# Kernel tuning notes

Measured on AMD Instinct MI355X. Metric: run time of the kernel, lower is better.

Reference implementation:

```python
import jax, jax.numpy as jnp
import numpy as np

B, N, D_IN, D_OUT, H, W = 2, 2048, 1024, 1024, 16, 64
DH = D_OUT // H


def setup_inputs() -> dict:
    key = jax.random.key(0)
    ks = jax.random.split(key, 6)
    x = jax.random.normal(ks[0], (B, N, D_IN), dtype=jnp.float32)
    s_in = 1.0 / np.sqrt(D_IN)
    s_out = 1.0 / np.sqrt(D_OUT)
    wq = jax.random.normal(ks[1], (D_IN, D_OUT), dtype=jnp.float32) * s_in
    wk = jax.random.normal(ks[2], (D_IN, D_OUT), dtype=jnp.float32) * s_in
    wv = jax.random.normal(ks[3], (D_IN, D_OUT), dtype=jnp.float32) * s_in
    wo = jax.random.normal(ks[4], (D_OUT, D_OUT), dtype=jnp.float32) * s_out
    # sparse global tokens: every 256th token is global
    global_attention = (jnp.arange(N)[None, :] % 256 == 0) & jnp.ones((B, 1), bool)
    return {"x": x, "wq": wq, "wk": wk, "wv": wv, "wo": wo,
            "global_attention": global_attention}


def _mask(global_attention):
    # True = masked out. Causal local window + global rows/cols unmasked.
    i = jnp.arange(N)[:, None]
    j = jnp.arange(N)[None, :]
    allowed = (i - j < W) & (i >= j)          # causal sliding window
    local_mask = ~allowed                      # [N, N], True = masked
    g = global_attention                       # [B, N] bool
    # global token j clears row j and column j of the mask
    global_clear = g[:, :, None] | g[:, None, :]   # [B, N, N]
    return local_mask[None, :, :] & ~global_clear  # [B, N, N]


def reference(x, wq, wk, wv, wo, global_attention):
    b, n, _ = x.shape
    q = (x @ wq).reshape(b, n, H, DH).transpose(0, 2, 1, 3)  # [b,h,n,dh]
    k = (x @ wk).reshape(b, n, H, DH).transpose(0, 2, 1, 3)
    v = (x @ wv).reshape(b, n, H, DH).transpose(0, 2, 1, 3)
    scores = jnp.einsum('bhqd,bhkd->bhqk', q, k) / jnp.sqrt(jnp.float32(DH))
    mask = _mask(global_attention)[:, None, :, :]            # [b,1,n,n]
    scores = jnp.where(mask, -jnp.inf, scores)
    attn = jax.nn.softmax(scores, axis=-1)
    ctx = jnp.einsum('bhqk,bhkd->bqhd', attn, v).reshape(b, n, D_OUT)
    return ctx @ wo
```

## Files before the change

### kernel.cpp

```cpp
#include <hip/hip_runtime.h>


using u16 = unsigned short;
using u32 = unsigned int;

typedef __attribute__((ext_vector_type(8))) short bf16x8;
typedef __attribute__((ext_vector_type(4))) float f32x4;

__device__ __forceinline__ float b2f(u16 s) {
  union { u32 u; float f; } x; x.u = ((u32)s) << 16; return x.f;
}
__device__ __forceinline__ u16 f2b(float f) {
  union { float f; u32 u; } x; x.f = f;
  u32 r = (x.u + 0x7fffu + ((x.u >> 16) & 1u)) >> 16;
  return (u16)r;
}

__global__ __launch_bounds__(256) void k_pre(const float* __restrict__ x,
                                             u16* __restrict__ xb,
                                             const float* __restrict__ wq,
                                             const float* __restrict__ wk,
                                             const float* __restrict__ wv,
                                             const float* __restrict__ wo,
                                             u16* __restrict__ wqkvT,
                                             u16* __restrict__ woT) {
  __shared__ float tile[64][65];
  const int bid = blockIdx.x;
  if (bid < 2048) {
    int idx = (bid * 256 + threadIdx.x) * 8;
    float4 a = *(const float4*)(x + idx);
    float4 b = *(const float4*)(x + idx + 4);
    uint4 o;
    o.x = (u32)f2b(a.x) | ((u32)f2b(a.y) << 16);
    o.y = (u32)f2b(a.z) | ((u32)f2b(a.w) << 16);
    o.z = (u32)f2b(b.x) | ((u32)f2b(b.y) << 16);
    o.w = (u32)f2b(b.z) | ((u32)f2b(b.w) << 16);
    *(uint4*)(xb + idx) = o;
  } else {
    const int id = bid - 2048;
    const int z = id >> 8, xy = id & 255;
    const float* src = (z == 0) ? wq : (z == 1) ? wk : (z == 2) ? wv : wo;
    u16* dst = (z < 3) ? (wqkvT + ((size_t)z << 20)) : woT;
    const int n0 = (xy & 15) * 64, k0 = (xy >> 4) * 64;
    const int tx = threadIdx.x & 63, ty = threadIdx.x >> 6;
    #pragma unroll
    for (int r = 0; r < 64; r += 4)
      tile[r + ty][tx] = src[(size_t)(k0 + r + ty) * 1024 + n0 + tx];
    __syncthreads();
    #pragma unroll
    for (int r = 0; r < 64; r += 4)
      dst[(size_t)(n0 + r + ty) * 1024 + k0 + tx] = f2b(tile[tx][r + ty]);
  }
}

__device__ __forceinline__ void gload16(const u16* g, u16* l) {
  __builtin_amdgcn_global_load_lds((const __attribute__((address_space(1))) void*)g,
                                   (__attribute__((address_space(3))) void*)l, 16, 0, 0);
}

template<int F32OUT>
__global__ __launch_bounds__(256, 3) void k_gemm128(const u16* __restrict__ A,
                                                    const u16* __restrict__ Bt,
                                                    void* __restrict__ C, int N, int K) {
  __shared__ u16 lds[3][2][4096];
  const int t = threadIdx.x;
  const int wid = t >> 6, lane = t & 63;
  const int l4 = lane >> 4, l16 = lane & 15;
  const int wr = wid >> 1, wc = wid & 1;
  const int d = blockIdx.y * gridDim.x + blockIdx.x;
  const int qq = (gridDim.x * gridDim.y) >> 3;
  const int tau = (d & 7) * qq + (d >> 3);
  const int bn = tau % gridDim.x, bm = tau / gridDim.x;
  const u16* Ab = A + (size_t)bm * 128 * K;
  const u16* Bb = Bt + (size_t)bn * 128 * K;
  const int srow0 = t >> 2;
  const int scol = (((t & 3) ^ ((t >> 3) & 3)) << 3);
  const int sdst = wid << 9;
  const int sl8 = ((l4 ^ ((l16 >> 1) & 3)) << 3);
  const int NT = K >> 5;
  f32x4 acc[4][4] = {};

  #pragma unroll
  for (int pt = 0; pt < 2; ++pt) {
    #pragma unroll
    for (int c = 0; c < 2; ++c) {
      int r = c * 64 + srow0;
      gload16(Ab + (size_t)r * K + (pt << 5) + scol, &lds[pt][0][c * 2048 + sdst]);
      gload16(Bb + (size_t)r * K + (pt << 5) + scol, &lds[pt][1][c * 2048 + sdst]);
    }
  }

  int cur = 0, nxt2 = 2;
  for (int tt = 0; tt < NT; ++tt) {
    if (tt + 1 < NT) asm volatile("s_waitcnt vmcnt(4)" ::: "memory");
    else             asm volatile("s_waitcnt vmcnt(0)" ::: "memory");
    __builtin_amdgcn_s_barrier();
    if (tt + 2 < NT) {
      const int k0 = (tt + 2) << 5;
      u16* dA = &lds[nxt2][0][sdst];
      u16* dB = &lds[nxt2][1][sdst];
      #pragma unroll
      for (int c = 0; c < 2; ++c) {
        int r = c * 64 + srow0;
        gload16(Ab + (size_t)r * K + k0 + scol, dA + c * 2048);
        gload16(Bb + (size_t)r * K + k0 + scol, dB + c * 2048);
      }
    }
    const u16* As = lds[cur][0];
    const u16* Bs = lds[cur][1];
    bf16x8 af[4], bf[4];
    #pragma unroll
    for (int m = 0; m < 4; ++m)
      af[m] = *(const bf16x8*)&As[(wr * 64 + m * 16 + l16) * 32 + sl8];
    #pragma unroll
    for (int n = 0; n < 4; ++n)
      bf[n] = *(const bf16x8*)&Bs[(wc * 64 + n * 16 + l16) * 32 + sl8];
    __builtin_amdgcn_s_setprio(1);
    #pragma unroll
    for (int m = 0; m < 4; ++m)
      #pragma unroll
      for (int n = 0; n < 4; ++n)
        acc[m][n] = __builtin_amdgcn_mfma_f32_16x16x32_bf16(af[m], bf[n], acc[m][n], 0, 0, 0);
    __builtin_amdgcn_s_setprio(0);
    cur = (cur == 2) ? 0 : cur + 1;
    nxt2 = (nxt2 == 2) ? 0 : nxt2 + 1;
  }

  #pragma unroll
  for (int m = 0; m < 4; ++m) {
    const int row0 = bm * 128 + wr * 64 + m * 16 + l4 * 4;
    #pragma unroll
    for (int n = 0; n < 4; ++n) {
      const int col = bn * 128 + wc * 64 + n * 16 + l16;
      #pragma unroll
      for (int r = 0; r < 4; ++r) {
        if (F32OUT) ((float*)C)[(size_t)(row0 + r) * N + col] = acc[m][n][r];
        else        ((u16*)C)[(size_t)(row0 + r) * N + col] = f2b(acc[m][n][r]);
      }
    }
  }
}

template<int F32OUT>
__global__ __launch_bounds__(256, 2) void k_gemm64(const u16* __restrict__ A,
                                                   const u16* __restrict__ Bt,
                                                   void* __restrict__ C, int N, int K) {
  __shared__ u16 lds[3][6144];
  const int t = threadIdx.x;
  const int wid = t >> 6, lane = t & 63;
  const int l4 = lane >> 4, l16 = lane & 15;
  const int wr = wid >> 1, wc = wid & 1;
  const int d = blockIdx.y * gridDim.x + blockIdx.x;
  const int qq = (gridDim.x * gridDim.y) >> 3;
  const int tau = (d & 7) * qq + (d >> 3);
  const int bn = tau % gridDim.x, bm = tau / gridDim.x;
  const u16* Ab = A + (size_t)bm * 64 * K;
  const u16* Bb = Bt + (size_t)bn * 128 * K;
  const int srow0 = t >> 2;
  const int scol = (((t & 3) ^ ((t >> 3) & 3)) << 3);
  const int sdst = wid << 9;
  const int sl8 = ((l4 ^ ((l16 >> 1) & 3)) << 3);
  const int NT = K >> 5;
  f32x4 acc[2][4] = {};

  #pragma unroll
  for (int pt = 0; pt < 2; ++pt) {
    gload16(Ab + (size_t)srow0 * K + (pt << 5) + scol, &lds[pt][sdst]);
    #pragma unroll
    for (int c = 0; c < 2; ++c)
      gload16(Bb + (size_t)(c * 64 + srow0) * K + (pt << 5) + scol,
              &lds[pt][2048 + c * 2048 + sdst]);
  }

  int cur = 0, nxt2 = 2;
  for (int tt = 0; tt < NT; ++tt) {
    if (tt + 1 < NT) asm volatile("s_waitcnt vmcnt(3)" ::: "memory");
    else             asm volatile("s_waitcnt vmcnt(0)" ::: "memory");
    __builtin_amdgcn_s_barrier();
    if (tt + 2 < NT) {
      const int k0 = (tt + 2) << 5;
      u16* dst = &lds[nxt2][0];
      gload16(Ab + (size_t)srow0 * K + k0 + scol, dst + sdst);
      #pragma unroll
      for (int c = 0; c < 2; ++c)
        gload16(Bb + (size_t)(c * 64 + srow0) * K + k0 + scol, dst + 2048 + c * 2048 + sdst);
    }
    const u16* As = lds[cur];
    const u16* Bs = lds[cur] + 2048;
    bf16x8 af[2], bf[4];
    #pragma unroll
    for (int m = 0; m < 2; ++m)
      af[m] = *(const bf16x8*)&As[(wr * 32 + m * 16 + l16) * 32 + sl8];
    #pragma unroll
    for (int n = 0; n < 4; ++n)
      bf[n] = *(const bf16x8*)&Bs[(wc * 64 + n * 16 + l16) * 32 + sl8];
    __builtin_amdgcn_s_setprio(1);
    #pragma unroll
    for (int m = 0; m < 2; ++m)
      #pragma unroll
      for (int n = 0; n < 4; ++n)
        acc[m][n] = __builtin_amdgcn_mfma_f32_16x16x32_bf16(af[m], bf[n], acc[m][n], 0, 0, 0);
    __builtin_amdgcn_s_setprio(0);
    cur = (cur == 2) ? 0 : cur + 1;
    nxt2 = (nxt2 == 2) ? 0 : nxt2 + 1;
  }

  #pragma unroll
  for (int m = 0; m < 2; ++m) {
    const int row0 = bm * 64 + wr * 32 + m * 16 + l4 * 4;
    #pragma unroll
    for (int n = 0; n < 4; ++n) {
      const int col = bn * 128 + wc * 64 + n * 16 + l16;
      #pragma unroll
      for (int r = 0; r < 4; ++r) {
        if (F32OUT) ((float*)C)[(size_t)(row0 + r) * N + col] = acc[m][n][r];
        else        ((u16*)C)[(size_t)(row0 + r) * N + col] = f2b(acc[m][n][r]);
      }
    }
  }
}

__global__ __launch_bounds__(256) void k_attn_tile(const u16* __restrict__ qkv,
                                                   u16* __restrict__ ctx,
                                                   float* __restrict__ gpart) {
  __shared__ u16 buf[26880];
  __shared__ u16 Qgs[16 * 72];
  __shared__ u16 Pgs[16 * 72];
  __shared__ float lred[4][16];
  u16* Qs = buf;
  u16* Ks = buf + 4608;
  u16* Vt = buf + 16128;
  u16* Ps = buf;

  const int t = threadIdx.x, wid = t >> 6, lane = t & 63;
  const int l4 = lane >> 4, l16 = lane & 15;
  const int qt = blockIdx.x, h = blockIdx.y, b = blockIdx.z;
  const int q0 = qt * 64;
  const int kbase = q0 - 64;
  const size_t base = (size_t)b * 2048 * 3072;
  const u16* Qg = qkv + base + h * 64;
  const u16* Kg = qkv + base + 1024 + h * 64;
  const u16* Vg = qkv + base + 2048 + h * 64;

  for (int s = t; s < 512; s += 256) {
    int r = s >> 3, c = (s & 7) * 8;
    *(uint4*)&Qs[r * 72 + c] = *(const uint4*)&Qg[(size_t)(q0 + r) * 3072 + c];
  }
  if (t < 128) {
    int r = t >> 3, c = (t & 7) * 8;
    if (r < 8) {
      *(uint4*)&Qgs[r * 72 + c] = *(const uint4*)&Qg[(size_t)(r * 256) * 3072 + c];
    } else {
      uint4 z = {0, 0, 0, 0};
      *(uint4*)&Qgs[r * 72 + c] = z;
    }
  }
  for (int s = t; s < 1088; s += 256) {
    int r = s >> 3, c = (s & 7) * 8;
    int j = (r < 128) ? max(kbase + r, 0) : (r - 128) * 256;
    *(uint4*)&Ks[r * 72 + c] = *(const uint4*)&Kg[(size_t)j * 3072 + c];
  }
  for (int s = t; s < 1088; s += 256) {
    int r = s >> 3, c = (s & 7) * 8;
    int j = (r < 128) ? max(kbase + r, 0) : (r - 128) * 256;
    uint4 v = *(const uint4*)&Vg[(size_t)j * 3072 + c];
    const u16* pv = (const u16*)&v;
    #pragma unroll
    for (int e8 = 0; e8 < 8; ++e8) Vt[(c + e8) * 168 + r] = pv[e8];
  }
  for (int z = t; z < 64 * 24; z += 256) {
    int d = z / 24, j = 136 + z % 24;
    Vt[d * 168 + j] = 0;
  }
  __syncthreads();

  f32x4 sa[10] = {};
  #pragma unroll
  for (int ks = 0; ks < 2; ++ks) {
    bf16x8 qa = *(const bf16x8*)&Qs[(wid * 16 + l16) * 72 + ks * 32 + l4 * 8];
    #pragma unroll
    for (int n = 0; n < 10; ++n) {
      bf16x8 kb = *(const bf16x8*)&Ks[(n * 16 + l16) * 72 + ks * 32 + l4 * 8];
      sa[n] = __builtin_amdgcn_mfma_f32_16x16x32_bf16(qa, kb, sa[n], 0, 0, 0);
    }
  }

  f32x4 sg = {};
  #pragma unroll
  for (int ks = 0; ks < 2; ++ks) {
    bf16x8 qa = *(const bf16x8*)&Qgs[l16 * 72 + ks * 32 + l4 * 8];
    bf16x8 kb = *(const bf16x8*)&Ks[(64 + wid * 16 + l16) * 72 + ks * 32 + l4 * 8];
    sg = __builtin_amdgcn_mfma_f32_16x16x32_bf16(qa, kb, sg, 0, 0, 0);
  }
  #pragma unroll
  for (int r = 0; r < 4; ++r) {
    float p = __expf(sg[r] * 0.125f);
    sg[r] = p;
    #pragma unroll
    for (int o = 1; o < 16; o <<= 1) p += __shfl_xor(p, o);
    if (l16 == 0) lred[wid][l4 * 4 + r] = p;
  }
  #pragma unroll
  for (int r = 0; r < 4; ++r)
    Pgs[(l4 * 4 + r) * 72 + wid * 16 + l16] = f2b(sg[r]);

  const int qi0 = wid * 16 + l4 * 4;
  #pragma unroll
  for (int n = 0; n < 10; ++n) {
    const int jc = n * 16 + l16;
    #pragma unroll
    for (int r = 0; r < 4; ++r) {
      const int qi = qi0 + r;
      bool allowed;
      if (n < 8) {
        const int kr = kbase + jc;
        allowed = (jc > qi) && (jc <= qi + 64) && (kr >= 0) && ((kr & 255) != 0);
      } else {
        allowed = (jc < 136);
      }
      sa[n][r] = allowed ? sa[n][r] * 0.125f : -1e30f;
    }
  }

  float m[4], l[4];
  #pragma unroll
  for (int r = 0; r < 4; ++r) {
    float mx = sa[0][r];
    #pragma unroll
    for (int n = 1; n < 10; ++n) mx = fmaxf(mx, sa[n][r]);
    #pragma unroll
    for (int o = 1; o < 16; o <<= 1) mx = fmaxf(mx, __shfl_xor(mx, o));
    m[r] = mx;
    l[r] = 0.f;
  }
  #pragma unroll
  for (int n = 0; n < 10; ++n)
    #pragma unroll
    for (int r = 0; r < 4; ++r) {
      float p = __expf(sa[n][r] - m[r]);
      sa[n][r] = p;
      l[r] += p;
    }
  #pragma unroll
  for (int r = 0; r < 4; ++r)
    #pragma unroll
    for (int o = 1; o < 16; o <<= 1) l[r] += __shfl_xor(l[r], o);

  __syncthreads();

  u16* Pw = Ps + wid * (16 * 168);
  #pragma unroll
  for (int n = 0; n < 10; ++n)
    #pragma unroll
    for (int r = 0; r < 4; ++r)
      Pw[(l4 * 4 + r) * 168 + n * 16 + l16] = f2b(sa[n][r]);
  __builtin_amdgcn_wave_barrier();

  f32x4 o[4] = {};
  #pragma unroll
  for (int ks = 0; ks < 5; ++ks) {
    bf16x8 pa = *(const bf16x8*)&Pw[l16 * 168 + ks * 32 + l4 * 8];
    #pragma unroll
    for (int dt = 0; dt < 4; ++dt) {
      bf16x8 vb = *(const bf16x8*)&Vt[(dt * 16 + l16) * 168 + ks * 32 + l4 * 8];
      o[dt] = __builtin_amdgcn_mfma_f32_16x16x32_bf16(pa, vb, o[dt], 0, 0, 0);
    }
  }

  f32x4 og = {};
  #pragma unroll
  for (int ks = 0; ks < 2; ++ks) {
    bf16x8 pa = *(const bf16x8*)&Pgs[l16 * 72 + ks * 32 + l4 * 8];
    bf16x8 vb = *(const bf16x8*)&Vt[(wid * 16 + l16) * 168 + 64 + ks * 32 + l4 * 8];
    og = __builtin_amdgcn_mfma_f32_16x16x32_bf16(pa, vb, og, 0, 0, 0);
  }
  float* gp = gpart + ((size_t)(b * 16 + h) * 32 + qt) * 520;
  #pragma unroll
  for (int r = 0; r < 4; ++r) {
    int row = l4 * 4 + r;
    if (row < 8) gp[row * 64 + wid * 16 + l16] = og[r];
  }
  if (t < 8) gp[512 + t] = lred[0][t] + lred[1][t] + lred[2][t] + lred[3][t];

  #pragma unroll
  for (int r = 0; r < 4; ++r) {
    const int q = q0 + qi0 + r;
    if ((q & 255) == 0) continue;
    const float inv = 1.0f / l[r];
    #pragma unroll
    for (int dt = 0; dt < 4; ++dt)
      ctx[(size_t)(b * 2048 + q) * 1024 + h * 64 + dt * 16 + l16] = f2b(o[dt][r] * inv);
  }
}

__global__ __launch_bounds__(256) void k_attn_gred(const float* __restrict__ gpart,
                                                   u16* __restrict__ ctx) {
  const int bh = blockIdx.x;
  const int b = bh >> 4, h = bh & 15;
  const float* gp0 = gpart + (size_t)bh * 32 * 520;
  for (int s = threadIdx.x; s < 512; s += 256) {
    int row = s >> 6, d = s & 63;
    float o = 0.f, l = 0.f;
    for (int q = 0; q < 32; ++q) {
      o += gp0[q * 520 + s];
      l += gp0[q * 520 + 512 + row];
    }
    ctx[(size_t)(b * 2048 + row * 256) * 1024 + h * 64 + d] = f2b(o / l);
  }
}

extern "C" void kernel_launch(void* const* d_in, const int* in_sizes, int n_in,
                              void* d_out, int out_size, void* d_ws, size_t ws_size,
                              hipStream_t stream) {
  (void)in_sizes; (void)n_in; (void)out_size; (void)ws_size;
  const float* x  = (const float*)d_in[0];
  const float* wq = (const float*)d_in[1];
  const float* wk = (const float*)d_in[2];
  const float* wv = (const float*)d_in[3];
  const float* wo = (const float*)d_in[4];
  char* ws = (char*)d_ws;
  u16* xb    = (u16*)(ws);
  u16* qkv   = (u16*)(ws + (8u  << 20));
  u16* ctx   = (u16*)(ws + (32u << 20));
  u16* wqkvT = (u16*)(ws + (40u << 20));
  u16* woT   = (u16*)(ws + (46u << 20));
  float* gpart = (float*)(ws);

  k_pre<<<3072, 256, 0, stream>>>(x, xb, wq, wk, wv, wo, wqkvT, woT);
  k_gemm128<0><<<dim3(24, 32), 256, 0, stream>>>(xb, wqkvT, qkv, 3072, 1024);
  k_attn_tile<<<dim3(32, 16, 2), 256, 0, stream>>>(qkv, ctx, gpart);
  k_attn_gred<<<32, 256, 0, stream>>>(gpart, ctx);
  k_gemm64<1><<<dim3(8, 64), 256, 0, stream>>>(ctx, woT, d_out, 1024, 1024);
}
```

Baseline: 89.26 us.

## Replace QKV GEMM with 256x256-tile, 8-wave kernel and quadrant-pipelined loads

New measurement: 90.05 us. About the same (+0.9%).

```diff
diff --git a/kernel.cpp b/kernel.cpp
--- a/kernel.cpp
+++ b/kernel.cpp
@@ -58,85 +58,127 @@
                                    (__attribute__((address_space(3))) void*)l, 16, 0, 0);
 }
 
-template<int F32OUT>
-__global__ __launch_bounds__(256, 3) void k_gemm128(const u16* __restrict__ A,
-                                                    const u16* __restrict__ Bt,
-                                                    void* __restrict__ C, int N, int K) {
-  __shared__ u16 lds[3][2][4096];
+__global__ __launch_bounds__(512, 2) void k_qkv256(const u16* __restrict__ A,
+                                                   const u16* __restrict__ Bt,
+                                                   u16* __restrict__ C, int N, int K) {
+  __shared__ __attribute__((aligned(16))) u16 lds[2][2][16384];
   const int t = threadIdx.x;
   const int wid = t >> 6, lane = t & 63;
   const int l4 = lane >> 4, l16 = lane & 15;
-  const int wr = wid >> 1, wc = wid & 1;
+  const int wr = wid >> 2, wc = wid & 3;
   const int d = blockIdx.y * gridDim.x + blockIdx.x;
   const int qq = (gridDim.x * gridDim.y) >> 3;
   const int tau = (d & 7) * qq + (d >> 3);
   const int bn = tau % gridDim.x, bm = tau / gridDim.x;
-  const u16* Ab = A + (size_t)bm * 128 * K;
-  const u16* Bb = Bt + (size_t)bn * 128 * K;
-  const int srow0 = t >> 2;
-  const int scol = (((t & 3) ^ ((t >> 3) & 3)) << 3);
-  const int sdst = wid << 9;
-  const int sl8 = ((l4 ^ ((l16 >> 1) & 3)) << 3);
-  const int NT = K >> 5;
-  f32x4 acc[4][4] = {};
-
-  #pragma unroll
-  for (int pt = 0; pt < 2; ++pt) {
-    #pragma unroll
-    for (int c = 0; c < 2; ++c) {
-      int r = c * 64 + srow0;
-      gload16(Ab + (size_t)r * K + (pt << 5) + scol, &lds[pt][0][c * 2048 + sdst]);
-      gload16(Bb + (size_t)r * K + (pt << 5) + scol, &lds[pt][1][c * 2048 + sdst]);
-    }
-  }
-
-  int cur = 0, nxt2 = 2;
+  const u16* Ab = A + (size_t)bm * 256 * K;
+  const u16* Bb = Bt + (size_t)bn * 256 * K;
+
+  int aoff[2], boff[2], dstoff[2];
+  #pragma unroll
+  for (int li = 0; li < 2; ++li) {
+    const int idx = li * 512 + wid * 64 + lane;
+    const int c8 = idx & 7;
+    const int jA = (idx >> 3) & 63;
+    aoff[li] = ((idx >> 9) * 128 + jA) * K + ((c8 ^ (jA & 7)) << 3);
+    const int j2 = (idx >> 3) & 31;
+    boff[li] = ((idx >> 8) * 64 + j2) * K + ((c8 ^ (j2 & 7)) << 3);
+    dstoff[li] = li * 4096 + wid * 512;
+  }
+
+  auto stageA = [&](int buf, int mh, int kt) {
+    const int g = mh * 64 * K + kt * 64;
+    #pragma unroll
+    for (int li = 0; li < 2; ++li)
+      gload16(Ab + aoff[li] + g, &lds[buf][0][mh * 8192 + dstoff[li]]);
+  };
+  auto stageB = [&](int buf, int nh, int kt) {
+    const int g = nh * 32 * K + kt * 64;
+    #pragma unroll
+    for (int li = 0; li < 2; ++li)
+      gload16(Bb + boff[li] + g, &lds[buf][1][nh * 8192 + dstoff[li]]);
+  };
+
+  const int baseA = (wr * 64 + l16) * 64;
+  const int baseB = (wc * 32 + l16) * 64;
+  const int sw0 = (l4 ^ (l16 & 7)) << 3;
+  const int sw1 = ((4 + l4) ^ (l16 & 7)) << 3;
+
+  bf16x8 af[4][2], bf[2][2][2];
+  f32x4 acc[8][4] = {};
+
+  auto loadA = [&](const u16* Ar, int mh) {
+    const u16* p = Ar + mh * 8192 + baseA;
+    #pragma unroll
+    for (int mp = 0; mp < 4; ++mp) {
+      af[mp][0] = *(const bf16x8*)(p + mp * 1024 + sw0);
+      af[mp][1] = *(const bf16x8*)(p + mp * 1024 + sw1);
+    }
+  };
+  auto loadB = [&](const u16* Br, int nh) {
+    const u16* p = Br + nh * 8192 + baseB;
+    #pragma unroll
+    for (int np = 0; np < 2; ++np) {
+      bf[nh][np][0] = *(const bf16x8*)(p + np * 1024 + sw0);
+      bf[nh][np][1] = *(const bf16x8*)(p + np * 1024 + sw1);
+    }
+  };
+  auto quad = [&](int mh, int nh) {
+    __builtin_amdgcn_s_setprio(1);
+    #pragma unroll
+    for (int mp = 0; mp < 4; ++mp)
+      #pragma unroll
+      for (int np = 0; np < 2; ++np) {
+        f32x4 c = acc[mh * 4 + mp][nh * 2 + np];
+        c = __builtin_amdgcn_mfma_f32_16x16x32_bf16(af[mp][0], bf[nh][np][0], c, 0, 0, 0);
+        c = __builtin_amdgcn_mfma_f32_16x16x32_bf16(af[mp][1], bf[nh][np][1], c, 0, 0, 0);
+        acc[mh * 4 + mp][nh * 2 + np] = c;
+      }
+    __builtin_amdgcn_s_setprio(0);
+  };
+
+  stageA(0, 0, 0); stageA(0, 1, 0); stageB(0, 0, 0); stageB(0, 1, 0);
+  stageA(1, 0, 1); stageB(1, 0, 1);
+  asm volatile("s_waitcnt vmcnt(4)" ::: "memory");
+  __builtin_amdgcn_s_barrier();
+
+  const int NT = K >> 6;
   for (int tt = 0; tt < NT; ++tt) {
-    if (tt + 1 < NT) asm volatile("s_waitcnt vmcnt(4)" ::: "memory");
+    const int buf = tt & 1;
+    const u16* Ar = lds[buf][0];
+    const u16* Br = lds[buf][1];
+    loadA(Ar, 0);
+    loadB(Br, 0);
+    if (tt + 1 < NT) stageA(buf ^ 1, 1, tt + 1);
+    __builtin_amdgcn_s_barrier();
+    quad(0, 0);
+    __builtin_amdgcn_s_barrier();
+    loadB(Br, 1);
+    if (tt + 1 < NT) stageB(buf ^ 1, 1, tt + 1);
+    __builtin_amdgcn_s_barrier();
+    quad(0, 1);
+    __builtin_amdgcn_s_barrier();
+    loadA(Ar, 1);
+    if (tt + 2 < NT) stageA(buf, 0, tt + 2);
+    __builtin_amdgcn_s_barrier();
+    quad(1, 0);
+    __builtin_amdgcn_s_barrier();
+    if (tt + 2 < NT) stageB(buf, 0, tt + 2);
+    __builtin_amdgcn_s_barrier();
+    quad(1, 1);
+    if (tt + 2 < NT) asm volatile("s_waitcnt vmcnt(4)" ::: "memory");
     else             asm volatile("s_waitcnt vmcnt(0)" ::: "memory");
     __builtin_amdgcn_s_barrier();
-    if (tt + 2 < NT) {
-      const int k0 = (tt + 2) << 5;
-      u16* dA = &lds[nxt2][0][sdst];
-      u16* dB = &lds[nxt2][1][sdst];
+  }
+
+  #pragma unroll
+  for (int m = 0; m < 8; ++m) {
+    const int row0 = bm * 256 + wr * 128 + m * 16 + l4 * 4;
+    #pragma unroll
+    for (int n = 0; n < 4; ++n) {
+      const int col = bn * 256 + wc * 64 + n * 16 + l16;
       #pragma unroll
-      for (int c = 0; c < 2; ++c) {
-        int r = c * 64 + srow0;
-        gload16(Ab + (size_t)r * K + k0 + scol, dA + c * 2048);
-        gload16(Bb + (size_t)r * K + k0 + scol, dB + c * 2048);
-      }
-    }
-    const u16* As = lds[cur][0];
-    const u16* Bs = lds[cur][1];
-    bf16x8 af[4], bf[4];
-    #pragma unroll
-    for (int m = 0; m < 4; ++m)
-      af[m] = *(const bf16x8*)&As[(wr * 64 + m * 16 + l16) * 32 + sl8];
-    #pragma unroll
-    for (int n = 0; n < 4; ++n)
-      bf[n] = *(const bf16x8*)&Bs[(wc * 64 + n * 16 + l16) * 32 + sl8];
-    __builtin_amdgcn_s_setprio(1);
-    #pragma unroll
-    for (int m = 0; m < 4; ++m)
-      #pragma unroll
-      for (int n = 0; n < 4; ++n)
-        acc[m][n] = __builtin_amdgcn_mfma_f32_16x16x32_bf16(af[m], bf[n], acc[m][n], 0, 0, 0);
-    __builtin_amdgcn_s_setprio(0);
-    cur = (cur == 2) ? 0 : cur + 1;
-    nxt2 = (nxt2 == 2) ? 0 : nxt2 + 1;
-  }
-
-  #pragma unroll
-  for (int m = 0; m < 4; ++m) {
-    const int row0 = bm * 128 + wr * 64 + m * 16 + l4 * 4;
-    #pragma unroll
-    for (int n = 0; n < 4; ++n) {
-      const int col = bn * 128 + wc * 64 + n * 16 + l16;
-      #pragma unroll
-      for (int r = 0; r < 4; ++r) {
-        if (F32OUT) ((float*)C)[(size_t)(row0 + r) * N + col] = acc[m][n][r];
-        else        ((u16*)C)[(size_t)(row0 + r) * N + col] = f2b(acc[m][n][r]);
-      }
+      for (int r = 0; r < 4; ++r)
+        C[(size_t)(row0 + r) * N + col] = f2b(acc[m][n][r]);
     }
   }
 }
@@ -427,7 +469,7 @@
   float* gpart = (float*)(ws);
 
   k_pre<<<3072, 256, 0, stream>>>(x, xb, wq, wk, wv, wo, wqkvT, woT);
-  k_gemm128<0><<<dim3(24, 32), 256, 0, stream>>>(xb, wqkvT, qkv, 3072, 1024);
+  k_qkv256<<<dim3(12, 16), 512, 0, stream>>>(xb, wqkvT, qkv, 3072, 1024);
   k_attn_tile<<<dim3(32, 16, 2), 256, 0, stream>>>(qkv, ctx, gpart);
   k_attn_gred<<<32, 256, 0, stream>>>(gpart, ctx);
   k_gemm64<1><<<dim3(8, 64), 256, 0, stream>>>(ctx, woT, d_out, 1024, 1024);
```
